# Optimization experiments

Measured on AMD Instinct MI355X. Metric: run time of the kernel, lower is better.

## Reference

```python
import jax, jax.numpy as jnp
import numpy as np

MU, LMBD = 1000.0, 5000.0
C1, C2 = 0.5, 0.5
SPACING = 1.0
EPS = 1e-8

# Cyclic minor indices: the 2x2 minor of entry (m,i) of a 3x3 matrix uses rows
# (m+1, m+2) mod 3 and cols (i+1, i+2) mod 3; det of that minor IS the signed
# cofactor (so minorSigns3d == ones, matching the original module's contract).
_r = (np.arange(3)[:, None, None, None] + 1 + np.arange(2)[None, None, :, None]) % 3
_c = (np.arange(3)[None, :, None, None] + 1 + np.arange(2)[None, None, None, :]) % 3
ROW_IDX = np.broadcast_to(_r, (3, 3, 2, 2))  # (m,i,p,q) -> row index into 3x3
COL_IDX = np.broadcast_to(_c, (3, 3, 2, 2))  # (m,i,p,q) -> col index into 3x3


def _cof2(M):
    # signed cofactor matrix of 2x2 matrices; M: (..., 2, 2)
    a, b = M[..., 0, 0], M[..., 0, 1]
    c, d = M[..., 1, 0], M[..., 1, 1]
    return jnp.stack([jnp.stack([d, -c], -1), jnp.stack([-b, a], -1)], -2)


def _div_pk1_neohook(gradU, hessU, mu, lmbd):
    # gradU: (b,i,j,k,3,3)  [d2=component, d1=spatial deriv]
    # hessU: (b,i,j,k,3,3,3) [d2, d1, d3]
    F = gradU + jnp.eye(3, dtype=gradU.dtype)
    idxF = F[..., ROW_IDX, COL_IDX]                                   # (...,3,3,2,2)
    cofF = idxF[..., 0, 0] * idxF[..., 1, 1] - idxF[..., 0, 1] * idxF[..., 1, 0]  # (...,3,3)
    idxHess = hessU[..., ROW_IDX, COL_IDX, :]                          # (...,3,3,2,2,3)
    # d/dx_j det(minor(F)[m,i]) = cof2(minor) : d(minor)/dx_j
    gradCofF = jnp.einsum('...mipq,...mipqj->...mij', _cof2(idxF), idxHess)
    F0, cofF0 = F[..., :, 0], cofF[..., :, 0]
    J = jnp.einsum('...m,...m->...', F0, cofF0) + EPS                  # det(F), col-0 expansion
    invJ = 1.0 / J
    gradJ = jnp.einsum('...m,...mj->...j', cofF0, hessU[..., :, 0, :]) \
          + jnp.einsum('...mj,...m->...j', gradCofF[..., :, 0, :], F0)
    divInvF_T = -jnp.einsum('...,...j,...mj->...m', invJ * invJ, gradJ, cofF) \
              + invJ[..., None] * jnp.einsum('...mjj->...m', gradCofF)
    divF = jnp.einsum('...mjj->...m', hessU)
    divPK1 = mu * (divF - divInvF_T)
    divPK1 = divPK1 + 0.5 * lmbd * (J * J - 1.0)[..., None] * divInvF_T
    divPK1 = divPK1 + lmbd * jnp.einsum('...ij,...j->...i', cofF, gradJ)
    return divPK1


def _phy_loss(pred):
    # pred: (b,i,j,k,3); central differences interior, one-sided at edges
    gradU = jnp.stack(jnp.gradient(pred, axis=(1, 2, 3)), axis=-1) / SPACING   # (b,i,j,k,3,3)
    hessU = jnp.stack(jnp.gradient(gradU, axis=(1, 2, 3)), axis=-1) / SPACING  # (b,i,j,k,3,3,3)
    r = _div_pk1_neohook(gradU, hessU, MU, LMBD)
    r = jnp.where(jnp.isnan(r), 0.0, r)  # r[r != r] = 0
    return jnp.mean(jnp.linalg.norm(r, axis=-1))


def setup_inputs() -> dict:
    key = jax.random.key(0)
    k1, k2 = jax.random.split(key)
    shape = (4, 64, 64, 64, 3)
    prediction = 0.01 * jax.random.normal(k1, shape, dtype=jnp.float32)
    target = 0.01 * jax.random.normal(k2, shape, dtype=jnp.float32)
    return {"prediction": prediction, "target": target}


def reference(prediction, target):
    mse_loss = jnp.mean((prediction - target) ** 2)
    phy_loss = _phy_loss(prediction)
    return C1 * mse_loss + C2 * phy_loss
```

## Files before the change

kernel.cpp:

```cpp
#include <hip/hip_runtime.h>
#include <math.h>

#define ND 64
#define NPTS (4 * ND * ND * ND)
#define SXG (ND * ND * 3)
#define SYG (ND * 3)

struct f3 { float v[3]; };

__device__ __forceinline__ f3 comb2(float a, const f3& X, float s, const f3& Y) {
    f3 r;
#pragma unroll
    for (int c = 0; c < 3; c++) r.v[c] = a * X.v[c] + s * Y.v[c];
    return r;
}
__device__ __forceinline__ f3 comb3(float a, const f3& X, float s, const f3& Y, float u, const f3& Z) {
    f3 r;
#pragma unroll
    for (int c = 0; c < 3; c++) r.v[c] = a * X.v[c] + s * Y.v[c] + u * Z.v[c];
    return r;
}

__device__ __forceinline__ float phys_norm(const float F[3][3], const float H[3][6]) {
    constexpr int SYM[3][3] = {{0, 3, 4}, {3, 1, 5}, {4, 5, 2}};

    float cof[3][3];
#pragma unroll
    for (int i = 0; i < 3; i++) {
        const int i1 = (i + 1) % 3, i2 = (i + 2) % 3;
#pragma unroll
        for (int j = 0; j < 3; j++) {
            const int j1 = (j + 1) % 3, j2 = (j + 2) % 3;
            cof[i][j] = F[i1][j1] * F[i2][j2] - F[i1][j2] * F[i2][j1];
        }
    }

    float gc0[3][3], trg[3];
#pragma unroll
    for (int m = 0; m < 3; m++) {
        const int m1 = (m + 1) % 3, m2 = (m + 2) % 3;
        trg[m] = 0.0f;
#pragma unroll
        for (int i = 0; i < 3; i++) {
            const int i1 = (i + 1) % 3, i2 = (i + 2) % 3;
#pragma unroll
            for (int j = 0; j < 3; j++) {
                if (i == 0 || i == j) {
                    const float g = F[m2][i2] * H[m1][SYM[i1][j]] + F[m1][i1] * H[m2][SYM[i2][j]]
                                  - F[m2][i1] * H[m1][SYM[i2][j]] - F[m1][i2] * H[m2][SYM[i1][j]];
                    if (i == 0) gc0[m][j] = g;
                    if (i == j) trg[m] += g;
                }
            }
        }
    }

    const float J = F[0][0] * cof[0][0] + F[1][0] * cof[1][0] + F[2][0] * cof[2][0] + 1e-8f;
    const float invJ = 1.0f / J;

    float gJ[3];
#pragma unroll
    for (int j = 0; j < 3; j++) {
        gJ[j] = cof[0][0] * H[0][SYM[0][j]] + cof[1][0] * H[1][SYM[0][j]] + cof[2][0] * H[2][SYM[0][j]]
              + gc0[0][j] * F[0][0] + gc0[1][j] * F[1][0] + gc0[2][j] * F[2][0];
    }

    const float MU = 1000.0f, LMBD = 5000.0f;
    const float halfL = 0.5f * LMBD * (J * J - 1.0f);
    float r[3];
#pragma unroll
    for (int m = 0; m < 3; m++) {
        const float s1 = gJ[0] * cof[m][0] + gJ[1] * cof[m][1] + gJ[2] * cof[m][2];
        const float divInv = -invJ * invJ * s1 + invJ * trg[m];
        const float divF = H[m][0] + H[m][1] + H[m][2];
        float v = MU * (divF - divInv) + halfL * divInv + LMBD * s1;
        r[m] = (v != v) ? 0.0f : v;
    }
    return sqrtf(r[0] * r[0] + r[1] * r[1] + r[2] * r[2]);
}

__device__ __forceinline__ void comp_row(
        float vC, float vXP, float vXM, float vYP, float vYM,
        float vXP2, float vXM2, float vYP2, float vYM2,
        float vPP, float vPM, float vMP, float vMM,
        int ip1, int im1, int ip2, int im2,
        bool l0, bool l1, bool l62, bool l63,
        float G[3], float Hr[6]) {
    const float d1r = __shfl(vC, ip1, 64), u1r = __shfl(vC, im1, 64);
    const float d2r = __shfl(vC, ip2, 64), u2r = __shfl(vC, im2, 64);
    const float d1 = l63 ? 2.f * vC - u1r : d1r;
    const float u1 = l0  ? 2.f * vC - d1r : u1r;
    const float d2 = l63 ? 4.f * vC - 4.f * u1r + u2r : (l62 ? 2.f * d1 - vC : d2r);
    const float u2 = l0  ? 4.f * vC - 4.f * d1r + d2r : (l1 ? 2.f * u1 - vC : u2r);

    float ad = __shfl(vXP, ip1, 64), au = __shfl(vXP, im1, 64);
    const float XPd = l63 ? 2.f * vXP - au : ad;
    const float XPu = l0  ? 2.f * vXP - ad : au;
    ad = __shfl(vXM, ip1, 64); au = __shfl(vXM, im1, 64);
    const float XMd = l63 ? 2.f * vXM - au : ad;
    const float XMu = l0  ? 2.f * vXM - ad : au;
    ad = __shfl(vYP, ip1, 64); au = __shfl(vYP, im1, 64);
    const float YPd = l63 ? 2.f * vYP - au : ad;
    const float YPu = l0  ? 2.f * vYP - ad : au;
    ad = __shfl(vYM, ip1, 64); au = __shfl(vYM, im1, 64);
    const float YMd = l63 ? 2.f * vYM - au : ad;
    const float YMu = l0  ? 2.f * vYM - ad : au;

    G[0] = 0.5f * (vXP - vXM);
    G[1] = 0.5f * (vYP - vYM);
    G[2] = 0.5f * (d1 - u1);
    Hr[0] = 0.25f * (vXP2 + vXM2) - 0.5f * vC;
    Hr[1] = 0.25f * (vYP2 + vYM2) - 0.5f * vC;
    Hr[2] = 0.25f * (d2 + u2) - 0.5f * vC;
    Hr[3] = 0.25f * ((vPP - vMP) - (vPM - vMM));
    Hr[4] = 0.25f * ((XPd - XMd) - (XPu - XMu));
    Hr[5] = 0.25f * ((YPd - YMd) - (YPu - YMu));
}

__global__ __launch_bounds__(512) void phys_loss_kernel(
        const float* __restrict__ pred,
        const float* __restrict__ targ,
        float* __restrict__ out) {
    const int t = threadIdx.x;
    const int lane = t & 63;
    const int wid = t >> 6;
    const int w = blockIdx.x * 8 + wid;
    const int y = w & 63;
    const int xseg = (w >> 6) & 7;
    const int b = w >> 9;
    const int z = lane;
    const int X0 = xseg * 8;

    const float* __restrict__ pb = pred + (size_t)b * (ND * SXG);
    const int yc1p = min(y + 1, 63), yc1m = max(y - 1, 0);
    const int yc2p = min(y + 2, 63), yc2m = max(y - 2, 0);

#define LDP(gx, gy) (*(const f3*)(pb + (size_t)((gx) * SXG + (gy) * SYG + z * 3)))

    auto fixy1 = [&](const f3& ypl, const f3& yml, const f3& cg, f3& ypc, f3& ymc) {
        if (y == 0)       { ypc = ypl; ymc = comb2(2.f, cg, -1.f, ypl); }
        else if (y == 63) { ymc = yml; ypc = comb2(2.f, cg, -1.f, yml); }
        else              { ypc = ypl; ymc = yml; }
    };
    auto fixy2 = [&](const f3& yp2l, const f3& ym2l, const f3& c0,
                     const f3& yp1, const f3& ym1, f3& o_p, f3& o_m) {
        if (y == 0)       { o_p = yp2l; o_m = comb3(4.f, c0, -4.f, yp1, 1.f, yp2l); }
        else if (y == 1)  { o_p = yp2l; o_m = comb2(2.f, ym1, -1.f, c0); }
        else if (y == 62) { o_m = ym2l; o_p = comb2(2.f, yp1, -1.f, c0); }
        else if (y == 63) { o_m = ym2l; o_p = comb3(4.f, c0, -4.f, ym1, 1.f, ym2l); }
        else              { o_p = yp2l; o_m = ym2l; }
    };

    f3 cc[5], cyp[3], cym[3], yp2, ym2;
    if (X0 == 0) {
        cc[2] = LDP(0, y); cc[3] = LDP(1, y); cc[4] = LDP(2, y);
        cc[1] = comb2(2.f, cc[2], -1.f, cc[3]);
        cc[0] = comb3(4.f, cc[2], -4.f, cc[3], 1.f, cc[4]);
        { f3 a = LDP(0, yc1p), bq = LDP(0, yc1m); fixy1(a, bq, cc[2], cyp[1], cym[1]); }
        { f3 a = LDP(1, yc1p), bq = LDP(1, yc1m); fixy1(a, bq, cc[3], cyp[2], cym[2]); }
        cyp[0] = comb2(2.f, cyp[1], -1.f, cyp[2]);
        cym[0] = comb2(2.f, cym[1], -1.f, cym[2]);
    } else {
#pragma unroll
        for (int k = 0; k < 5; k++) cc[k] = LDP(X0 - 2 + k, y);
#pragma unroll
        for (int k = 0; k < 3; k++) {
            f3 a = LDP(X0 - 1 + k, yc1p), bq = LDP(X0 - 1 + k, yc1m);
            fixy1(a, bq, cc[k + 1], cyp[k], cym[k]);
        }
    }
    { f3 a = LDP(X0, yc2p), bq = LDP(X0, yc2m);
      fixy2(a, bq, cc[2], cyp[1], cym[1], yp2, ym2); }

    const bool l0 = (z == 0), l1 = (z == 1), l62 = (z == 62), l63 = (z == 63);
    const int ip1 = (lane + 1) & 63, im1 = (lane + 63) & 63;
    const int ip2 = (lane + 2) & 63, im2 = (lane + 62) & 63;

    float accn = 0.f, accs = 0.f;

#pragma unroll 2
    for (int i = 0; i < 8; i++) {
        const int x0 = X0 + i;

        f3 cin, ypin, ymin, yp2in, ym2in;
        if (i < 7) {
            const int gxc = min(x0 + 3, 63);
            const int gx1 = min(x0 + 2, 63);
            cin  = LDP(gxc, y);
            ypin = LDP(gx1, yc1p);  ymin = LDP(gx1, yc1m);
            yp2in = LDP(x0 + 1, yc2p);  ym2in = LDP(x0 + 1, yc2m);
        }
        const f3 T = *(const f3*)(targ + (size_t)b * (ND * SXG)
                                  + (size_t)(x0 * SXG + y * SYG + z * 3));

        float F[3][3], H[3][6], G[3];
        comp_row(cc[2].v[0], cc[3].v[0], cc[1].v[0], cyp[1].v[0], cym[1].v[0],
                 cc[4].v[0], cc[0].v[0], yp2.v[0], ym2.v[0],
                 cyp[2].v[0], cym[2].v[0], cyp[0].v[0], cym[0].v[0],
                 ip1, im1, ip2, im2, l0, l1, l62, l63, G, H[0]);
        F[0][0] = G[0] + 1.f; F[0][1] = G[1]; F[0][2] = G[2];
        comp_row(cc[2].v[1], cc[3].v[1], cc[1].v[1], cyp[1].v[1], cym[1].v[1],
                 cc[4].v[1], cc[0].v[1], yp2.v[1], ym2.v[1],
                 cyp[2].v[1], cym[2].v[1], cyp[0].v[1], cym[0].v[1],
                 ip1, im1, ip2, im2, l0, l1, l62, l63, G, H[1]);
        F[1][0] = G[0]; F[1][1] = G[1] + 1.f; F[1][2] = G[2];
        comp_row(cc[2].v[2], cc[3].v[2], cc[1].v[2], cyp[1].v[2], cym[1].v[2],
                 cc[4].v[2], cc[0].v[2], yp2.v[2], ym2.v[2],
                 cyp[2].v[2], cym[2].v[2], cyp[0].v[2], cym[0].v[2],
                 ip1, im1, ip2, im2, l0, l1, l62, l63, G, H[2]);
        F[2][0] = G[0]; F[2][1] = G[1]; F[2][2] = G[2] + 1.f;

        accn += phys_norm(F, H);

        const float dx = cc[2].v[0] - T.v[0];
        const float dy = cc[2].v[1] - T.v[1];
        const float dz = cc[2].v[2] - T.v[2];
        accs += dx * dx + dy * dy + dz * dz;

        if (i < 7) {
            cc[0] = cc[1]; cc[1] = cc[2]; cc[2] = cc[3]; cc[3] = cc[4];
            cyp[0] = cyp[1]; cyp[1] = cyp[2];
            cym[0] = cym[1]; cym[1] = cym[2];
            const int nx0 = x0 + 1;
            if (nx0 + 2 <= 63)      cc[4] = cin;
            else if (nx0 + 2 == 64) cc[4] = comb2(2.f, cc[3], -1.f, cc[2]);
            else                    cc[4] = comb3(4.f, cc[2], -4.f, cc[1], 1.f, cc[0]);
            if (nx0 + 1 <= 63) {
                fixy1(ypin, ymin, cc[3], cyp[2], cym[2]);
            } else {
                cyp[2] = comb2(2.f, cyp[1], -1.f, cyp[0]);
                cym[2] = comb2(2.f, cym[1], -1.f, cym[0]);
            }
            fixy2(yp2in, ym2in, cc[2], cyp[1], cym[1], yp2, ym2);
        }
    }
#undef LDP

    const float invN = 1.0f / (float)NPTS;
    float val = 0.5f * accs * (invN * (1.0f / 3.0f)) + 0.5f * accn * invN;

#pragma unroll
    for (int off = 32; off > 0; off >>= 1) val += __shfl_down(val, off, 64);

    __shared__ float wsum[8];
    if (lane == 0) wsum[wid] = val;
    __syncthreads();
    if (t == 0) {
        float acc = 0.0f;
#pragma unroll
        for (int wq = 0; wq < 8; wq++) acc += wsum[wq];
        atomicAdd(out, acc);
    }
}

extern "C" void kernel_launch(void* const* d_in, const int* in_sizes, int n_in,
                              void* d_out, int out_size, void* d_ws, size_t ws_size,
                              hipStream_t stream) {
    const float* pred = (const float*)d_in[0];
    const float* targ = (const float*)d_in[1];
    float* out = (float*)d_out;

    hipMemsetAsync(out, 0, sizeof(float), stream);

    const int blocks = 256;
    phys_loss_kernel<<<blocks, 512, 0, stream>>>(pred, targ, out);
}
```

Before: 32.36 us.

## Halve x-segment length per wave and derive mixed z-derivatives from gradients

Each wavefront now processes 4 x-rows instead of 8, doubling the grid to spread work across more CUs, with the per-segment loop fully unrolled. The mixed xz/yz second derivatives are now computed by shuffling the already-formed x/y central differences along z, cutting the shuffle count per component. The shorter segments increase redundant halo loads in the prologue relative to useful work.

After: 33.90 us. 4.8% more time.

```diff
diff --git a/kernel.cpp b/kernel.cpp
--- a/kernel.cpp
+++ b/kernel.cpp
@@ -5,6 +5,7 @@
 #define NPTS (4 * ND * ND * ND)
 #define SXG (ND * ND * 3)
 #define SYG (ND * 3)
+#define XSEG 4
 
 struct f3 { float v[3]; };
 
@@ -93,28 +94,19 @@
     const float d2 = l63 ? 4.f * vC - 4.f * u1r + u2r : (l62 ? 2.f * d1 - vC : d2r);
     const float u2 = l0  ? 4.f * vC - 4.f * d1r + d2r : (l1 ? 2.f * u1 - vC : u2r);
 
-    float ad = __shfl(vXP, ip1, 64), au = __shfl(vXP, im1, 64);
-    const float XPd = l63 ? 2.f * vXP - au : ad;
-    const float XPu = l0  ? 2.f * vXP - ad : au;
-    ad = __shfl(vXM, ip1, 64); au = __shfl(vXM, im1, 64);
-    const float XMd = l63 ? 2.f * vXM - au : ad;
-    const float XMu = l0  ? 2.f * vXM - ad : au;
-    ad = __shfl(vYP, ip1, 64); au = __shfl(vYP, im1, 64);
-    const float YPd = l63 ? 2.f * vYP - au : ad;
-    const float YPu = l0  ? 2.f * vYP - ad : au;
-    ad = __shfl(vYM, ip1, 64); au = __shfl(vYM, im1, 64);
-    const float YMd = l63 ? 2.f * vYM - au : ad;
-    const float YMu = l0  ? 2.f * vYM - ad : au;
-
-    G[0] = 0.5f * (vXP - vXM);
-    G[1] = 0.5f * (vYP - vYM);
-    G[2] = 0.5f * (d1 - u1);
+    const float g0 = 0.5f * (vXP - vXM);
+    const float g1 = 0.5f * (vYP - vYM);
+    G[0] = g0; G[1] = g1; G[2] = 0.5f * (d1 - u1);
+
+    const float g0d = __shfl(g0, ip1, 64), g0u = __shfl(g0, im1, 64);
+    const float g1d = __shfl(g1, ip1, 64), g1u = __shfl(g1, im1, 64);
+
     Hr[0] = 0.25f * (vXP2 + vXM2) - 0.5f * vC;
     Hr[1] = 0.25f * (vYP2 + vYM2) - 0.5f * vC;
     Hr[2] = 0.25f * (d2 + u2) - 0.5f * vC;
     Hr[3] = 0.25f * ((vPP - vMP) - (vPM - vMM));
-    Hr[4] = 0.25f * ((XPd - XMd) - (XPu - XMu));
-    Hr[5] = 0.25f * ((YPd - YMd) - (YPu - YMu));
+    Hr[4] = 0.5f * ((l63 ? 2.f * g0 - g0u : g0d) - (l0 ? 2.f * g0 - g0d : g0u));
+    Hr[5] = 0.5f * ((l63 ? 2.f * g1 - g1u : g1d) - (l0 ? 2.f * g1 - g1d : g1u));
 }
 
 __global__ __launch_bounds__(512) void phys_loss_kernel(
@@ -126,10 +118,10 @@
     const int wid = t >> 6;
     const int w = blockIdx.x * 8 + wid;
     const int y = w & 63;
-    const int xseg = (w >> 6) & 7;
-    const int b = w >> 9;
+    const int xseg = (w >> 6) & 15;
+    const int b = w >> 10;
     const int z = lane;
-    const int X0 = xseg * 8;
+    const int X0 = xseg * XSEG;
 
     const float* __restrict__ pb = pred + (size_t)b * (ND * SXG);
     const int yc1p = min(y + 1, 63), yc1m = max(y - 1, 0);
@@ -178,12 +170,12 @@
 
     float accn = 0.f, accs = 0.f;
 
-#pragma unroll 2
-    for (int i = 0; i < 8; i++) {
+#pragma unroll
+    for (int i = 0; i < XSEG; i++) {
         const int x0 = X0 + i;
 
         f3 cin, ypin, ymin, yp2in, ym2in;
-        if (i < 7) {
+        if (i < XSEG - 1) {
             const int gxc = min(x0 + 3, 63);
             const int gx1 = min(x0 + 2, 63);
             cin  = LDP(gxc, y);
@@ -217,7 +209,7 @@
         const float dz = cc[2].v[2] - T.v[2];
         accs += dx * dx + dy * dy + dz * dz;
 
-        if (i < 7) {
+        if (i < XSEG - 1) {
             cc[0] = cc[1]; cc[1] = cc[2]; cc[2] = cc[3]; cc[3] = cc[4];
             cyp[0] = cyp[1]; cyp[1] = cyp[2];
             cym[0] = cym[1]; cym[1] = cym[2];
@@ -262,6 +254,6 @@
 
     hipMemsetAsync(out, 0, sizeof(float), stream);
 
-    const int blocks = 256;
+    const int blocks = (4 * 64 * (64 / XSEG)) / 8;
     phys_loss_kernel<<<blocks, 512, 0, stream>>>(pred, targ, out);
 }
```
